# Optimization experiments

Hardware: AMD Instinct MI355X
Metric: run time of the kernel (lower is better)

## Reference

```python
import jax, jax.numpy as jnp
import numpy as np
from jax import lax

STRIDES = (8, 8, 16, 32, 32)
GRIDS = (40, 36, 24, 16, 12)
MIN_SCORE = 0.1
KEEP_SCORE = 0.1
MASK_THR = 0.5
UPDATE_THR = 0.05
SIGMA = 2.0
TOPN = 500
MAX_MASKS = 100
UP = 4


def points_nms(h):
    # max_pool2d(k=2, s=1, p=1) then crop last row/col == pad (1,0) window 2
    m = lax.reduce_window(h, -jnp.inf, lax.max, (1, 1, 2, 2), (1, 1, 1, 1),
                          ((0, 0), (0, 0), (1, 0), (1, 0)))
    return h * (m == h).astype(h.dtype)


def resize_mat(insz, outsz):
    # bilinear align_corners=True interpolation matrix [outsz, insz]
    if outsz > 1:
        src = jnp.arange(outsz, dtype=jnp.float32) * ((insz - 1) / (outsz - 1))
    else:
        src = jnp.zeros((outsz,), jnp.float32)
    lo = jnp.clip(jnp.floor(src).astype(jnp.int32), 0, insz - 1)
    hi = jnp.minimum(lo + 1, insz - 1)
    w = src - lo.astype(jnp.float32)
    r = jnp.arange(outsz)
    M = jnp.zeros((outsz, insz), jnp.float32)
    return M.at[r, lo].add(1.0 - w).at[r, hi].add(w)


def bilinear(x, oh, ow):  # x: [k,h,w]
    Mh = resize_mat(x.shape[1], oh)
    Mw = resize_mat(x.shape[2], ow)
    return jnp.einsum('Ww,kHw->kHW', Mw, jnp.einsum('Hh,khw->kHw', Mh, x))


def prep(cate_preds, kernel_preds):
    B = cate_preds[0].shape[0]
    cate = [points_nms(jax.nn.sigmoid(c)) for c in cate_preds]
    cate_flat = jnp.concatenate(
        [jnp.transpose(c, (0, 2, 3, 1)).reshape(B, -1, c.shape[1]) for c in cate], axis=1)
    kern_flat = jnp.concatenate(
        [jnp.transpose(k, (0, 2, 3, 1)).reshape(B, -1, k.shape[1]) for k in kernel_preds], axis=1)
    strides_vec = jnp.concatenate(
        [jnp.full((g * g,), float(s), jnp.float32) for g, s in zip(GRIDS, STRIDES)])
    return cate_flat, kern_flat, strides_vec


def decode_soft(mask_feat, cate_flat, kern_flat, strides_vec):
    # fixed-shape (padded) version of the per-image decode; invalid slots carry score 0
    nc = cate_flat.shape[-1]
    flat = cate_flat.reshape(-1)
    vals, idx = lax.top_k(jnp.where(flat > MIN_SCORE, flat, -1.0), TOPN)
    validk = vals > MIN_SCORE
    cell = idx // nc
    label = idx % nc
    # dynamic 1x1 conv == einsum with gathered kernels
    sig = jax.nn.sigmoid(jnp.einsum('kc,chw->khw', kern_flat[cell], mask_feat))
    binm = (sig > MASK_THR).astype(sig.dtype)
    summ = binm.sum((1, 2))
    keep = validk & (summ > strides_vec[cell])
    seg = (sig * binm).sum((1, 2)) / jnp.maximum(summ, 1e-6)
    scores = jnp.where(keep, vals * seg, 0.0)
    order = jnp.argsort(-scores)
    scores = scores[order]
    sig = sig[order]
    label = label[order]
    keep_o = keep[order]
    summ = jnp.where(keep, summ, 0.0)[order]
    binm = binm[order] * keep_o[:, None, None].astype(binm.dtype)
    # matrix NMS (gaussian)
    flatm = binm.reshape(TOPN, -1)
    inter = flatm @ flatm.T
    iou = inter / jnp.maximum(summ[:, None] + summ[None, :] - inter, 1e-6)
    triu = jnp.triu(jnp.ones((TOPN, TOPN), bool), 1)
    dmat = jnp.where(triu & (label[:, None] == label[None, :]), iou, 0.0)
    comp = dmat.max(0)  # max suppression each item received
    coef = (jnp.exp(-SIGMA * dmat**2) / jnp.exp(-SIGMA * comp[:, None]**2)).min(0)
    s2 = scores * coef
    s2 = jnp.where((s2 >= UPDATE_THR) & (s2 >= KEEP_SCORE) & keep_o, s2, 0.0)
    fv, fi = lax.top_k(s2, MAX_MASKS)
    return fv, jnp.where(fv > 0, label[fi], -1), sig[fi]


def reference(mask_feat_pred, cate_pred_0, cate_pred_1, cate_pred_2, cate_pred_3,
              cate_pred_4, kernel_pred_0, kernel_pred_1, kernel_pred_2, kernel_pred_3,
              kernel_pred_4, scaled_sizes, origin_sizes):
    cate_preds = [cate_pred_0, cate_pred_1, cate_pred_2, cate_pred_3, cate_pred_4]
    kernel_preds = [kernel_pred_0, kernel_pred_1, kernel_pred_2, kernel_pred_3, kernel_pred_4]
    cate_flat, kern_flat, sv = prep(cate_preds, kernel_preds)
    fv, lab, sig = jax.vmap(lambda mf, cf, kf: decode_soft(mf, cf, kf, sv))(
        mask_feat_pred, cate_flat, kern_flat)
    H = mask_feat_pred.shape[2] * UP
    W = mask_feat_pred.shape[3] * UP
    up = jax.vmap(lambda s: bilinear(s, H, W))(sig)  # [B,M,H,W]
    sh, sw = int(scaled_sizes[0, 0]), int(scaled_sizes[0, 1])
    oh, ow = int(origin_sizes[0, 0]), int(origin_sizes[0, 1])
    up = up[:, :, :sh, :sw]
    up = jax.vmap(lambda s: bilinear(s, oh, ow))(up)
    masks = ((up > MASK_THR) & (fv > 0)[:, :, None, None]).astype(jnp.uint8)
    return masks, lab, fv


def setup_inputs() -> dict:
    key = jax.random.key(0)
    ks = jax.random.split(key, 11)
    B, C, NC, HM = 2, 256, 80, 128
    inp = {'mask_feat_pred': jax.random.normal(ks[0], (B, C, HM, HM), jnp.float32)}
    for i, g in enumerate(GRIDS):
        inp[f'cate_pred_{i}'] = jax.random.normal(ks[1 + i], (B, NC, g, g), jnp.float32)
        inp[f'kernel_pred_{i}'] = jax.random.normal(ks[6 + i], (B, C, g, g), jnp.float32) * 0.05
    inp['scaled_sizes'] = jnp.full((B, 2), HM * UP, jnp.int32)
    inp['origin_sizes'] = jnp.full((B, 2), HM * UP, jnp.int32)
    return inp
```

## Files before the change

### kernel.cpp

```cpp
#include <hip/hip_runtime.h>
#include <math.h>
#include <stdint.h>

#define NBATCH 2
#define NC 80
#define CHN 256
#define HMM 128
#define HWN (HMM*HMM)
#define NCELL 3872
#define FLATN (NCELL*NC)
#define TOPN 500
#define SROWS 512
#define MAXM 100
#define OUTH 512
#define OUTW 512
#define NBINS 1024
#define CANDCAP 1024
#define BM 128
#define BN 128
#define BK 16
#define GNB (HWN/BN)

__device__ __forceinline__ float sigmoidf_(float x){ return 1.0f/(1.0f+expf(-x)); }

__device__ __forceinline__ void cell_decode(int cell, int& lvl, int& g, int& y, int& x){
  int off;
  if (cell < 1600)      { lvl=0; g=40; off=0; }
  else if (cell < 2896) { lvl=1; g=36; off=1600; }
  else if (cell < 3472) { lvl=2; g=24; off=2896; }
  else if (cell < 3728) { lvl=3; g=16; off=3472; }
  else                  { lvl=4; g=12; off=3728; }
  int r = cell - off; y = r / g; x = r - y*g;
}

template<int N, int NT>
__device__ __forceinline__ void bitonic_desc(uint64_t* key){
  int tid = threadIdx.x;
  __syncthreads();
  for (int k = 2; k <= N; k <<= 1)
    for (int j = k >> 1; j > 0; j >>= 1) {
      if (j >= 32) __syncthreads();
      for (int e = tid; e < N; e += NT) {
        int l = e ^ j;
        if (l > e) {
          uint64_t a = key[e], c = key[l];
          bool up = ((e & k) == 0);
          if (up ? (a < c) : (a > c)) { key[e] = c; key[l] = a; }
        }
      }
    }
  __syncthreads();
}

__global__ void k1_scores(const float* __restrict__ c0, const float* __restrict__ c1,
                          const float* __restrict__ c2, const float* __restrict__ c3,
                          const float* __restrict__ c4,
                          float* __restrict__ scores_t, uint32_t* __restrict__ hist){
  int t = blockIdx.x*blockDim.x + threadIdx.x;
  if (t >= NBATCH*FLATN) return;
  int b = t / FLATN;
  int rem = t - b*FLATN;
  int c = rem / NCELL;
  int cell = rem - c*NCELL;
  int lvl,g,y,x; cell_decode(cell,lvl,g,y,x);
  const float* cp = lvl==0?c0:lvl==1?c1:lvl==2?c2:lvl==3?c3:c4;
  const float* base = cp + (size_t)(b*NC + c)*g*g;
  float raw = base[y*g + x];
  float m = raw;
  if (y > 0)          m = fmaxf(m, base[(y-1)*g + x]);
  if (x > 0)          m = fmaxf(m, base[y*g + x-1]);
  if (y > 0 && x > 0) m = fmaxf(m, base[(y-1)*g + x-1]);
  float s = (raw == m) ? sigmoidf_(raw) : 0.0f;
  scores_t[t] = s;
  if (s > 0.1f) {
    int bin = (int)(s * 1024.0f); if (bin > NBINS-1) bin = NBINS-1;
    atomicAdd(&hist[b*NBINS + bin], 1u);
  }
}

__global__ __launch_bounds__(1024) void k2_cutoff(const uint32_t* __restrict__ hist, int* __restrict__ cutoff){
  __shared__ uint32_t h[NBINS];
  int b = blockIdx.x;
  h[threadIdx.x] = hist[b*NBINS + threadIdx.x];
  __syncthreads();
  if (threadIdx.x == 0) {
    int acc = 0; int cut = 0;
    for (int d = NBINS-1; d >= 0; --d) {
      acc += (int)h[d];
      if (acc >= TOPN) { cut = d; break; }
    }
    cutoff[b] = cut;
  }
}

__global__ void k3_gather(const float* __restrict__ scores_t, const int* __restrict__ cutoff,
                          uint32_t* __restrict__ cnt, float* __restrict__ cval, uint32_t* __restrict__ cidx){
  int t = blockIdx.x*blockDim.x + threadIdx.x;
  if (t >= NBATCH*FLATN) return;
  int b = t / FLATN;
  int rem = t - b*FLATN;
  int c = rem / NCELL;
  int cell = rem - c*NCELL;
  float v = scores_t[t];
  if (v > 0.1f) {
    int bin = (int)(v * 1024.0f); if (bin > NBINS-1) bin = NBINS-1;
    if (bin >= cutoff[b]) {
      uint32_t p = atomicAdd(&cnt[b], 1u);
      if (p < CANDCAP) { cval[b*CANDCAP+p] = v; cidx[b*CANDCAP+p] = (uint32_t)(cell*NC + c); }
    }
  }
}

__global__ __launch_bounds__(512) void k4_sort(const uint32_t* __restrict__ cnt,
        const float* __restrict__ cval, const uint32_t* __restrict__ cidx,
        float* __restrict__ vals, int* __restrict__ cellA, int* __restrict__ labelA){
  __shared__ uint64_t key[CANDCAP];
  int b = blockIdx.x; int tid = threadIdx.x;
  int n = (int)cnt[b]; if (n > CANDCAP) n = CANDCAP;
  for (int e = tid; e < CANDCAP; e += 512) {
    uint64_t k = 0;
    if (e < n)
      k = ((uint64_t)__float_as_uint(cval[b*CANDCAP+e]) << 32) |
          (uint64_t)(0xFFFFFFFFu - cidx[b*CANDCAP+e]);
    key[e] = k;
  }
  bitonic_desc<CANDCAP,512>(key);
  for (int r = tid; r < TOPN; r += 512) {
    uint64_t k = key[r];
    if ((k >> 32) == 0) { vals[b*TOPN+r] = -1.0f; cellA[b*TOPN+r] = 0; labelA[b*TOPN+r] = 0; }
    else {
      uint32_t idx = 0xFFFFFFFFu - (uint32_t)(k & 0xFFFFFFFFu);
      vals[b*TOPN+r]   = __uint_as_float((uint32_t)(k >> 32));
      cellA[b*TOPN+r]  = (int)(idx / NC);
      labelA[b*TOPN+r] = (int)(idx % NC);
    }
  }
}

__global__ void k5_kmat(const float* __restrict__ k0p, const float* __restrict__ k1p,
                        const float* __restrict__ k2p, const float* __restrict__ k3p,
                        const float* __restrict__ k4p,
                        const int* __restrict__ cellA, float* __restrict__ Kmat){
  int t = blockIdx.x*blockDim.x + threadIdx.x;
  if (t >= NBATCH*TOPN*CHN) return;
  int b = t / (TOPN*CHN); int rem = t - b*(TOPN*CHN);
  int k = rem / CHN; int c = rem - k*CHN;
  int cell = cellA[b*TOPN + k];
  int lvl,g,y,x; cell_decode(cell,lvl,g,y,x);
  const float* kp = lvl==0?k0p:lvl==1?k1p:lvl==2?k2p:lvl==3?k3p:k4p;
  Kmat[t] = kp[((size_t)(b*CHN + c)*g + y)*g + x];
}

__global__ __launch_bounds__(256) void k6_gemm1(const float* __restrict__ Kmat, const float* __restrict__ mf,
        float* __restrict__ sigfull, uint32_t* __restrict__ bits,
        float* __restrict__ psum, float* __restrict__ pseg){
  __shared__ alignas(16) float As[2][BK][BM+4];
  __shared__ alignas(16) float Bs[2][BK][BN];
  int tid = threadIdx.x;
  int nb = blockIdx.x, mb = blockIdx.y, b = blockIdx.z;
  int row0 = mb*BM, col0 = nb*BN;
  int tx = tid & 15, ty = tid >> 4;

  int ar[2], aq[2], bkk[2], bcc[2];
  #pragma unroll
  for (int i = 0; i < 2; ++i) {
    int e = i*256 + tid;
    ar[i] = e >> 2; aq[i] = e & 3;
    bkk[i] = e >> 5; bcc[i] = e & 31;
  }
  float4 pa[2], pb[2];
  const float4 z4 = make_float4(0.f,0.f,0.f,0.f);
  #pragma unroll
  for (int i = 0; i < 2; ++i) {
    int rr = row0 + ar[i];
    pa[i] = (rr < TOPN) ? *(const float4*)&Kmat[((size_t)b*TOPN + rr)*CHN + aq[i]*4] : z4;
    pb[i] = *(const float4*)&mf[((size_t)b*CHN + bkk[i])*HWN + col0 + bcc[i]*4];
  }
  #pragma unroll
  for (int i = 0; i < 2; ++i) {
    int colA = ar[i] ^ (aq[i] << 2);
    As[0][aq[i]*4+0][colA] = pa[i].x;
    As[0][aq[i]*4+1][colA] = pa[i].y;
    As[0][aq[i]*4+2][colA] = pa[i].z;
    As[0][aq[i]*4+3][colA] = pa[i].w;
    *(float4*)&Bs[0][bkk[i]][bcc[i]*4] = pb[i];
  }
  __syncthreads();

  float acc[8][8];
  #pragma unroll
  for (int i=0;i<8;i++)
    #pragma unroll
    for(int j=0;j<8;j++) acc[i][j]=0.f;

  int cur = 0;
  for (int k0 = 0; k0 < CHN; k0 += BK) {
    bool more = (k0 + BK < CHN);
    if (more) {
      int k0n = k0 + BK;
      #pragma unroll
      for (int i = 0; i < 2; ++i) {
        int rr = row0 + ar[i];
        pa[i] = (rr < TOPN) ? *(const float4*)&Kmat[((size_t)b*TOPN + rr)*CHN + k0n + aq[i]*4] : z4;
        pb[i] = *(const float4*)&mf[((size_t)b*CHN + k0n + bkk[i])*HWN + col0 + bcc[i]*4];
      }
    }
    #pragma unroll 4
    for (int kk = 0; kk < BK; ++kk) {
      int s = (kk >> 2) << 2;
      float4 a0 = *(float4*)&As[cur][kk][(ty*8) ^ s];
      float4 a1 = *(float4*)&As[cur][kk][(ty*8+4) ^ s];
      float4 b0 = *(float4*)&Bs[cur][kk][tx*4];
      float4 b1 = *(float4*)&Bs[cur][kk][64+tx*4];
      float av[8] = {a0.x,a0.y,a0.z,a0.w,a1.x,a1.y,a1.z,a1.w};
      #pragma unroll
      for (int i = 0; i < 8; ++i) {
        acc[i][0] += av[i]*b0.x; acc[i][1] += av[i]*b0.y; acc[i][2] += av[i]*b0.z; acc[i][3] += av[i]*b0.w;
        acc[i][4] += av[i]*b1.x; acc[i][5] += av[i]*b1.y; acc[i][6] += av[i]*b1.z; acc[i][7] += av[i]*b1.w;
      }
    }
    if (more) {
      int nxt = cur ^ 1;
      #pragma unroll
      for (int i = 0; i < 2; ++i) {
        int colA = ar[i] ^ (aq[i] << 2);
        As[nxt][aq[i]*4+0][colA] = pa[i].x;
        As[nxt][aq[i]*4+1][colA] = pa[i].y;
        As[nxt][aq[i]*4+2][colA] = pa[i].z;
        As[nxt][aq[i]*4+3][colA] = pa[i].w;
        *(float4*)&Bs[nxt][bkk[i]][bcc[i]*4] = pb[i];
      }
      __syncthreads();
      cur = nxt;
    }
  }
  #pragma unroll
  for (int i = 0; i < 8; ++i) {
    int r = row0 + ty*8 + i;
    float se = 0.f; int cc = 0;
    #pragma unroll
    for (int q = 0; q < 2; ++q) {
      float4 sv;
      sv.x = sigmoidf_(acc[i][q*4+0]);
      sv.y = sigmoidf_(acc[i][q*4+1]);
      sv.z = sigmoidf_(acc[i][q*4+2]);
      sv.w = sigmoidf_(acc[i][q*4+3]);
      uint32_t m = 0;
      if (sv.x > 0.5f) { m |= 1u; se += sv.x; cc++; }
      if (sv.y > 0.5f) { m |= 2u; se += sv.y; cc++; }
      if (sv.z > 0.5f) { m |= 4u; se += sv.z; cc++; }
      if (sv.w > 0.5f) { m |= 8u; se += sv.w; cc++; }
      uint32_t wrd = m << ((tx & 7)*4);
      wrd |= __shfl_xor(wrd, 1);
      wrd |= __shfl_xor(wrd, 2);
      wrd |= __shfl_xor(wrd, 4);
      if ((tx & 7) == 0 && r < TOPN)
        bits[((size_t)b*TOPN + r)*512 + nb*4 + q*2 + (tx>>3)] = wrd;
      *(float4*)&sigfull[((size_t)b*SROWS + r)*HWN + col0 + q*64 + tx*4] = sv;
    }
    #pragma unroll
    for (int d = 1; d < 16; d <<= 1) {
      se += __shfl_xor(se, d);
      cc += __shfl_xor(cc, d);
    }
    if (tx == 0 && r < TOPN) {
      psum[((size_t)b*TOPN + r)*GNB + nb] = (float)cc;
      pseg[((size_t)b*TOPN + r)*GNB + nb] = se;
    }
  }
}

__global__ __launch_bounds__(512) void k78_stats_order(const float* __restrict__ psum, const float* __restrict__ pseg,
        const float* __restrict__ vals, const int* __restrict__ cellA,
        float* __restrict__ summ, float* __restrict__ scores, int* __restrict__ keepA,
        int* __restrict__ order, float* __restrict__ comp){
  __shared__ uint64_t key[512];
  int b = blockIdx.x, tid = threadIdx.x;
  uint64_t k = 0;
  if (tid < TOPN) {
    int t = b*TOPN + tid;
    comp[t] = 0.f;
    float sc = 0.f, sg = 0.f;
    for (int i = 0; i < GNB; i += 4) {
      float4 a = *(const float4*)&psum[(size_t)t*GNB+i];
      float4 c = *(const float4*)&pseg[(size_t)t*GNB+i];
      sc += a.x+a.y+a.z+a.w; sg += c.x+c.y+c.z+c.w;
    }
    float v = vals[t];
    int cell = cellA[t];
    int lvl,g,y,x; cell_decode(cell,lvl,g,y,x);
    float stride = (lvl<=1)?8.f:(lvl==2)?16.f:32.f;
    bool keep = (v > 0.1f) && (sc > stride);
    float seg = sg / fmaxf(sc, 1e-6f);
    summ[t] = sc;
    float s = keep ? v*seg : 0.f;
    scores[t] = s;
    keepA[t] = keep ? 1 : 0;
    k = ((uint64_t)__float_as_uint(s) << 32) | (uint64_t)(0xFFFFFFFFu - (uint32_t)tid);
  }
  key[tid] = k;
  bitonic_desc<512,512>(key);
  if (tid < TOPN) order[b*TOPN+tid] = (int)(0xFFFFFFFFu - (uint32_t)(key[tid] & 0xFFFFFFFFu));
}

__global__ __launch_bounds__(256) void k9_dmat(const uint32_t* __restrict__ bitsG,
        const int* __restrict__ order, const int* __restrict__ labelA, const int* __restrict__ keepA,
        const float* __restrict__ summ, float* __restrict__ dmatT, float* __restrict__ comp){
  __shared__ uint32_t rowb[512];
  int i = blockIdx.x, b = blockIdx.y, tid = threadIdx.x;
  int oi = order[b*TOPN + i];
  if (!keepA[b*TOPN + oi]) return;
  float si = summ[b*TOPN + oi];
  int li = labelA[b*TOPN + oi];
  for (int w = tid; w < 512; w += 256) rowb[w] = bitsG[((size_t)b*TOPN + oi)*512 + w];
  __syncthreads();
  for (int j = i + 1 + tid; j < TOPN; j += 256) {
    int oj = order[b*TOPN + j];
    if (!keepA[b*TOPN + oj] || labelA[b*TOPN + oj] != li) continue;
    const uint4* rj = (const uint4*)&bitsG[((size_t)b*TOPN + oj)*512];
    const uint4* ri = (const uint4*)rowb;
    int cc = 0;
    for (int w = 0; w < 128; ++w) {
      uint4 x = rj[w], y = ri[w];
      cc += __popc(x.x & y.x) + __popc(x.y & y.y) + __popc(x.z & y.z) + __popc(x.w & y.w);
    }
    float sj = summ[b*TOPN + oj];
    float inter = (float)cc;
    float v = inter / fmaxf(si + sj - inter, 1e-6f);
    dmatT[((size_t)b*TOPN + j)*TOPN + i] = v;
    if (v > 0.f) atomicMax((int*)&comp[b*TOPN + j], __float_as_int(v));
  }
}

__global__ __launch_bounds__(256) void k10_coef(const float* __restrict__ dmatT, const float* __restrict__ comp,
        const float* __restrict__ scores, const int* __restrict__ order, const int* __restrict__ keepA,
        float* __restrict__ s2){
  __shared__ float red[4];
  int j = blockIdx.x, b = blockIdx.y, tid = threadIdx.x;
  float mn = 1e30f;
  for (int i = tid; i < TOPN; i += 256) {
    float d = dmatT[((size_t)b*TOPN+j)*TOPN + i];
    float c = comp[b*TOPN+i];
    float r = expf(-2.0f*d*d) / expf(-2.0f*c*c);
    mn = fminf(mn, r);
  }
  #pragma unroll
  for (int d = 1; d < 64; d <<= 1) mn = fminf(mn, __shfl_xor(mn, d));
  if ((tid & 63) == 0) red[tid >> 6] = mn;
  __syncthreads();
  if (tid == 0) {
    mn = fminf(fminf(red[0], red[1]), fminf(red[2], red[3]));
    int oj = order[b*TOPN+j];
    float s = scores[b*TOPN+oj] * mn;
    bool ok = (s >= 0.05f) && (s >= 0.1f) && (keepA[b*TOPN+oj] != 0);
    s2[b*TOPN+j] = ok ? s : 0.f;
  }
}

__global__ __launch_bounds__(512) void k11_top100(const float* __restrict__ s2, const int* __restrict__ order,
        const int* __restrict__ labelA, float* __restrict__ outF, int* __restrict__ selrow){
  __shared__ uint64_t key[512];
  int b = blockIdx.x, tid = threadIdx.x;
  uint64_t k = 0;
  if (tid < TOPN)
    k = ((uint64_t)__float_as_uint(s2[b*TOPN+tid]) << 32) | (uint64_t)(0xFFFFFFFFu - (uint32_t)tid);
  key[tid] = k;
  bitonic_desc<512,512>(key);
  if (tid < MAXM) {
    uint64_t kk = key[tid];
    float v = __uint_as_float((uint32_t)(kk >> 32));
    int j = (int)(0xFFFFFFFFu - (uint32_t)(kk & 0xFFFFFFFFu));
    if (j < 0 || j >= TOPN) { j = 0; v = 0.f; }
    int orow = order[b*TOPN + j];
    float lab = (v > 0.f) ? (float)labelA[b*TOPN + orow] : -1.0f;
    size_t maskCount = (size_t)NBATCH*MAXM*OUTH*OUTW;
    outF[maskCount + (size_t)b*MAXM + tid] = lab;
    outF[maskCount + (size_t)NBATCH*MAXM + (size_t)b*MAXM + tid] = v;
    selrow[b*MAXM + tid] = orow;
  }
}

__global__ void k13_upsample(const float* __restrict__ sigfull, const int* __restrict__ selrow,
                             float* __restrict__ outF){
  int t = blockIdx.x*blockDim.x + threadIdx.x;
  const int XG = OUTW/4;
  int total = NBATCH*MAXM*OUTH*XG;
  if (t >= total) return;
  int xg = t % XG;
  int tmp = t / XG;
  int Y = tmp % OUTH;
  int tmp2 = tmp / OUTH;
  int r = tmp2 % MAXM;
  int b = tmp2 / MAXM;
  size_t maskCount = (size_t)NBATCH*MAXM*OUTH*OUTW;
  float fv = outF[maskCount + (size_t)NBATCH*MAXM + (size_t)b*MAXM + r];
  float4 o = make_float4(0.f,0.f,0.f,0.f);
  if (fv > 0.f) {
    const float* sm = sigfull + ((size_t)b*SROWS + selrow[b*MAXM + r])*HWN;
    const float SC = (float)(127.0/511.0);
    float fy = (float)Y * SC;
    int ly = (int)floorf(fy); if (ly < 0) ly = 0; if (ly > HMM-1) ly = HMM-1;
    int hy = ly+1 < HMM ? ly+1 : HMM-1;
    float wy = fy - (float)ly;
    float res[4];
    #pragma unroll
    for (int u = 0; u < 4; ++u) {
      int X = xg*4 + u;
      float fx = (float)X * SC;
      int lx = (int)floorf(fx); if (lx < 0) lx = 0; if (lx > HMM-1) lx = HMM-1;
      int hx = lx+1 < HMM ? lx+1 : HMM-1;
      float wx = fx - (float)lx;
      float a = (1.f-wy)*sm[ly*HMM+lx] + wy*sm[hy*HMM+lx];
      float c = (1.f-wy)*sm[ly*HMM+hx] + wy*sm[hy*HMM+hx];
      float v = (1.f-wx)*a + wx*c;
      res[u] = (v > 0.5f) ? 1.f : 0.f;
    }
    o = make_float4(res[0],res[1],res[2],res[3]);
  }
  *(float4*)&outF[(((size_t)b*MAXM + r)*OUTH + Y)*OUTW + xg*4] = o;
}

extern "C" void kernel_launch(void* const* d_in, const int* in_sizes, int n_in,
                              void* d_out, int out_size, void* d_ws, size_t ws_size,
                              hipStream_t stream) {
  const float* mf = (const float*)d_in[0];
  const float *cate[5], *kern[5];
  bool interleaved = (n_in > 2) && (in_sizes[2] == NBATCH*CHN*40*40);
  if (interleaved) {
    for (int i = 0; i < 5; ++i) { cate[i] = (const float*)d_in[1 + 2*i]; kern[i] = (const float*)d_in[2 + 2*i]; }
  } else {
    for (int i = 0; i < 5; ++i) { cate[i] = (const float*)d_in[1 + i]; kern[i] = (const float*)d_in[6 + i]; }
  }
  float* outF = (float*)d_out;

  uint8_t* p = (uint8_t*)d_ws;
  auto alloc = [&](size_t bytes) -> void* {
    void* r = (void*)p;
    p += (bytes + 255) & ~(size_t)255;
    return r;
  };
  float*    scores_t    = (float*)   alloc((size_t)NBATCH*FLATN*4);
  uint32_t* hist        = (uint32_t*)alloc((size_t)(NBATCH*NBINS + NBATCH)*4);
  uint32_t* cnt         = hist + NBATCH*NBINS;
  int*      cutoff      = (int*)     alloc((size_t)NBATCH*4);
  float*    cval        = (float*)   alloc((size_t)NBATCH*CANDCAP*4);
  uint32_t* cidx        = (uint32_t*)alloc((size_t)NBATCH*CANDCAP*4);
  float*    vals        = (float*)   alloc((size_t)NBATCH*TOPN*4);
  int*      cellA       = (int*)     alloc((size_t)NBATCH*TOPN*4);
  int*      labelA      = (int*)     alloc((size_t)NBATCH*TOPN*4);
  float*    Kmat        = (float*)   alloc((size_t)NBATCH*TOPN*CHN*4);
  uint32_t* bits        = (uint32_t*)alloc((size_t)NBATCH*TOPN*512*4);
  float*    psum        = (float*)   alloc((size_t)NBATCH*TOPN*GNB*4);
  float*    pseg        = (float*)   alloc((size_t)NBATCH*TOPN*GNB*4);
  float*    summ        = (float*)   alloc((size_t)NBATCH*TOPN*4);
  float*    scores      = (float*)   alloc((size_t)NBATCH*TOPN*4);
  int*      keepA       = (int*)     alloc((size_t)NBATCH*TOPN*4);
  int*      order       = (int*)     alloc((size_t)NBATCH*TOPN*4);
  float*    dmatT       = (float*)   alloc((size_t)NBATCH*TOPN*TOPN*4);
  float*    comp        = (float*)   alloc((size_t)NBATCH*TOPN*4);
  float*    s2          = (float*)   alloc((size_t)NBATCH*TOPN*4);
  int*      selrow      = (int*)     alloc((size_t)NBATCH*MAXM*4);
  float*    sigfull     = (float*)   alloc((size_t)NBATCH*SROWS*HWN*4);
  (void)ws_size; (void)out_size;

  hipMemsetAsync(hist, 0, (size_t)(NBATCH*NBINS + NBATCH)*4, stream);
  hipMemsetAsync(dmatT, 0, (size_t)NBATCH*TOPN*TOPN*4, stream);
  hipLaunchKernelGGL(k1_scores, dim3((NBATCH*FLATN + 255)/256), dim3(256), 0, stream,
                     cate[0], cate[1], cate[2], cate[3], cate[4], scores_t, hist);
  hipLaunchKernelGGL(k2_cutoff, dim3(NBATCH), dim3(1024), 0, stream, hist, cutoff);
  hipLaunchKernelGGL(k3_gather, dim3((NBATCH*FLATN + 255)/256), dim3(256), 0, stream,
                     scores_t, cutoff, cnt, cval, cidx);
  hipLaunchKernelGGL(k4_sort, dim3(NBATCH), dim3(512), 0, stream, cnt, cval, cidx, vals, cellA, labelA);
  hipLaunchKernelGGL(k5_kmat, dim3((NBATCH*TOPN*CHN + 255)/256), dim3(256), 0, stream,
                     kern[0], kern[1], kern[2], kern[3], kern[4], cellA, Kmat);
  hipLaunchKernelGGL(k6_gemm1, dim3(GNB, (TOPN+BM-1)/BM, NBATCH), dim3(256), 0, stream,
                     Kmat, mf, sigfull, bits, psum, pseg);
  hipLaunchKernelGGL(k78_stats_order, dim3(NBATCH), dim3(512), 0, stream,
                     psum, pseg, vals, cellA, summ, scores, keepA, order, comp);
  hipLaunchKernelGGL(k9_dmat, dim3(TOPN, NBATCH), dim3(256), 0, stream,
                     bits, order, labelA, keepA, summ, dmatT, comp);
  hipLaunchKernelGGL(k10_coef, dim3(TOPN, NBATCH), dim3(256), 0, stream,
                     dmatT, comp, scores, order, keepA, s2);
  hipLaunchKernelGGL(k11_top100, dim3(NBATCH), dim3(512), 0, stream, s2, order, labelA, outF, selrow);
  hipLaunchKernelGGL(k13_upsample, dim3((NBATCH*MAXM*OUTH*(OUTW/4) + 255)/256), dim3(256), 0, stream,
                     sigfull, selrow, outF);
}
```

Baseline: 385.7 us.

## Store sigmoid masks as bf16, transpose partial sums, merge workspace memsets

The full-resolution sigmoid buffer written by the GEMM and read by the upsample kernel is stored as bf16 instead of fp32, halving that large intermediate's write and read traffic. The per-block partial count and sum arrays are transposed so the stats kernel reads them coalesced across threads. The two zeroing memsets are merged into one by placing the histogram and distance matrix next to each other. The bf16 rounding can flip mask pixels whose interpolated value lies near the 0.5 threshold.

New measurement: 375.1 us. 2.7% less time.

```diff
diff --git a/kernel.cpp b/kernel.cpp
--- a/kernel.cpp
+++ b/kernel.cpp
@@ -22,6 +22,12 @@
 #define GNB (HWN/BN)
 
 __device__ __forceinline__ float sigmoidf_(float x){ return 1.0f/(1.0f+expf(-x)); }
+__device__ __forceinline__ unsigned short f2bf(float x){
+  uint32_t u = __float_as_uint(x);
+  uint32_t r = u + 0x7FFFu + ((u >> 16) & 1u);
+  return (unsigned short)(r >> 16);
+}
+__device__ __forceinline__ float bf2f(unsigned short h){ return __uint_as_float(((uint32_t)h) << 16); }
 
 __device__ __forceinline__ void cell_decode(int cell, int& lvl, int& g, int& y, int& x){
   int off;
@@ -152,7 +158,7 @@
 }
 
 __global__ __launch_bounds__(256) void k6_gemm1(const float* __restrict__ Kmat, const float* __restrict__ mf,
-        float* __restrict__ sigfull, uint32_t* __restrict__ bits,
+        unsigned short* __restrict__ sigb, uint32_t* __restrict__ bits,
         float* __restrict__ psum, float* __restrict__ pseg){
   __shared__ alignas(16) float As[2][BK][BM+4];
   __shared__ alignas(16) float Bs[2][BK][BN];
@@ -256,7 +262,9 @@
       wrd |= __shfl_xor(wrd, 4);
       if ((tx & 7) == 0 && r < TOPN)
         bits[((size_t)b*TOPN + r)*512 + nb*4 + q*2 + (tx>>3)] = wrd;
-      *(float4*)&sigfull[((size_t)b*SROWS + r)*HWN + col0 + q*64 + tx*4] = sv;
+      ushort4 sb;
+      sb.x = f2bf(sv.x); sb.y = f2bf(sv.y); sb.z = f2bf(sv.z); sb.w = f2bf(sv.w);
+      *(ushort4*)&sigb[((size_t)b*SROWS + r)*HWN + col0 + q*64 + tx*4] = sb;
     }
     #pragma unroll
     for (int d = 1; d < 16; d <<= 1) {
@@ -264,8 +272,8 @@
       cc += __shfl_xor(cc, d);
     }
     if (tx == 0 && r < TOPN) {
-      psum[((size_t)b*TOPN + r)*GNB + nb] = (float)cc;
-      pseg[((size_t)b*TOPN + r)*GNB + nb] = se;
+      psum[(size_t)nb*(NBATCH*TOPN) + b*TOPN + r] = (float)cc;
+      pseg[(size_t)nb*(NBATCH*TOPN) + b*TOPN + r] = se;
     }
   }
 }
@@ -281,10 +289,9 @@
     int t = b*TOPN + tid;
     comp[t] = 0.f;
     float sc = 0.f, sg = 0.f;
-    for (int i = 0; i < GNB; i += 4) {
-      float4 a = *(const float4*)&psum[(size_t)t*GNB+i];
-      float4 c = *(const float4*)&pseg[(size_t)t*GNB+i];
-      sc += a.x+a.y+a.z+a.w; sg += c.x+c.y+c.z+c.w;
+    for (int i = 0; i < GNB; ++i) {
+      sc += psum[(size_t)i*(NBATCH*TOPN) + t];
+      sg += pseg[(size_t)i*(NBATCH*TOPN) + t];
     }
     float v = vals[t];
     int cell = cellA[t];
@@ -380,7 +387,7 @@
   }
 }
 
-__global__ void k13_upsample(const float* __restrict__ sigfull, const int* __restrict__ selrow,
+__global__ void k13_upsample(const unsigned short* __restrict__ sigb, const int* __restrict__ selrow,
                              float* __restrict__ outF){
   int t = blockIdx.x*blockDim.x + threadIdx.x;
   const int XG = OUTW/4;
@@ -396,7 +403,7 @@
   float fv = outF[maskCount + (size_t)NBATCH*MAXM + (size_t)b*MAXM + r];
   float4 o = make_float4(0.f,0.f,0.f,0.f);
   if (fv > 0.f) {
-    const float* sm = sigfull + ((size_t)b*SROWS + selrow[b*MAXM + r])*HWN;
+    const unsigned short* sm = sigb + ((size_t)b*SROWS + selrow[b*MAXM + r])*HWN;
     const float SC = (float)(127.0/511.0);
     float fy = (float)Y * SC;
     int ly = (int)floorf(fy); if (ly < 0) ly = 0; if (ly > HMM-1) ly = HMM-1;
@@ -410,8 +417,8 @@
       int lx = (int)floorf(fx); if (lx < 0) lx = 0; if (lx > HMM-1) lx = HMM-1;
       int hx = lx+1 < HMM ? lx+1 : HMM-1;
       float wx = fx - (float)lx;
-      float a = (1.f-wy)*sm[ly*HMM+lx] + wy*sm[hy*HMM+lx];
-      float c = (1.f-wy)*sm[ly*HMM+hx] + wy*sm[hy*HMM+hx];
+      float a = (1.f-wy)*bf2f(sm[ly*HMM+lx]) + wy*bf2f(sm[hy*HMM+lx]);
+      float c = (1.f-wy)*bf2f(sm[ly*HMM+hx]) + wy*bf2f(sm[hy*HMM+hx]);
       float v = (1.f-wx)*a + wx*c;
       res[u] = (v > 0.5f) ? 1.f : 0.f;
     }
@@ -439,9 +446,13 @@
     p += (bytes + 255) & ~(size_t)255;
     return r;
   };
-  float*    scores_t    = (float*)   alloc((size_t)NBATCH*FLATN*4);
+  uint8_t*  zbase       = p;
   uint32_t* hist        = (uint32_t*)alloc((size_t)(NBATCH*NBINS + NBATCH)*4);
   uint32_t* cnt         = hist + NBATCH*NBINS;
+  float*    dmatT       = (float*)   alloc((size_t)NBATCH*TOPN*TOPN*4);
+  size_t    zbytes      = (size_t)(p - zbase);
+
+  float*    scores_t    = (float*)   alloc((size_t)NBATCH*FLATN*4);
   int*      cutoff      = (int*)     alloc((size_t)NBATCH*4);
   float*    cval        = (float*)   alloc((size_t)NBATCH*CANDCAP*4);
   uint32_t* cidx        = (uint32_t*)alloc((size_t)NBATCH*CANDCAP*4);
@@ -450,21 +461,19 @@
   int*      labelA      = (int*)     alloc((size_t)NBATCH*TOPN*4);
   float*    Kmat        = (float*)   alloc((size_t)NBATCH*TOPN*CHN*4);
   uint32_t* bits        = (uint32_t*)alloc((size_t)NBATCH*TOPN*512*4);
-  float*    psum        = (float*)   alloc((size_t)NBATCH*TOPN*GNB*4);
-  float*    pseg        = (float*)   alloc((size_t)NBATCH*TOPN*GNB*4);
+  float*    psum        = (float*)   alloc((size_t)GNB*NBATCH*TOPN*4);
+  float*    pseg        = (float*)   alloc((size_t)GNB*NBATCH*TOPN*4);
   float*    summ        = (float*)   alloc((size_t)NBATCH*TOPN*4);
   float*    scores      = (float*)   alloc((size_t)NBATCH*TOPN*4);
   int*      keepA       = (int*)     alloc((size_t)NBATCH*TOPN*4);
   int*      order       = (int*)     alloc((size_t)NBATCH*TOPN*4);
-  float*    dmatT       = (float*)   alloc((size_t)NBATCH*TOPN*TOPN*4);
   float*    comp        = (float*)   alloc((size_t)NBATCH*TOPN*4);
   float*    s2          = (float*)   alloc((size_t)NBATCH*TOPN*4);
   int*      selrow      = (int*)     alloc((size_t)NBATCH*MAXM*4);
-  float*    sigfull     = (float*)   alloc((size_t)NBATCH*SROWS*HWN*4);
+  unsigned short* sigb  = (unsigned short*)alloc((size_t)NBATCH*SROWS*HWN*2);
   (void)ws_size; (void)out_size;
 
-  hipMemsetAsync(hist, 0, (size_t)(NBATCH*NBINS + NBATCH)*4, stream);
-  hipMemsetAsync(dmatT, 0, (size_t)NBATCH*TOPN*TOPN*4, stream);
+  hipMemsetAsync(zbase, 0, zbytes, stream);
   hipLaunchKernelGGL(k1_scores, dim3((NBATCH*FLATN + 255)/256), dim3(256), 0, stream,
                      cate[0], cate[1], cate[2], cate[3], cate[4], scores_t, hist);
   hipLaunchKernelGGL(k2_cutoff, dim3(NBATCH), dim3(1024), 0, stream, hist, cutoff);
@@ -474,7 +483,7 @@
   hipLaunchKernelGGL(k5_kmat, dim3((NBATCH*TOPN*CHN + 255)/256), dim3(256), 0, stream,
                      kern[0], kern[1], kern[2], kern[3], kern[4], cellA, Kmat);
   hipLaunchKernelGGL(k6_gemm1, dim3(GNB, (TOPN+BM-1)/BM, NBATCH), dim3(256), 0, stream,
-                     Kmat, mf, sigfull, bits, psum, pseg);
+                     Kmat, mf, sigb, bits, psum, pseg);
   hipLaunchKernelGGL(k78_stats_order, dim3(NBATCH), dim3(512), 0, stream,
                      psum, pseg, vals, cellA, summ, scores, keepA, order, comp);
   hipLaunchKernelGGL(k9_dmat, dim3(TOPN, NBATCH), dim3(256), 0, stream,
@@ -483,5 +492,5 @@
                      dmatT, comp, scores, order, keepA, s2);
   hipLaunchKernelGGL(k11_top100, dim3(NBATCH), dim3(512), 0, stream, s2, order, labelA, outF, selrow);
   hipLaunchKernelGGL(k13_upsample, dim3((NBATCH*MAXM*OUTH*(OUTW/4) + 255)/256), dim3(256), 0, stream,
-                     sigfull, selrow, outF);
-}
+                     sigb, selrow, outF);
+}
```
